# Kernel optimization log

Measured on AMD Instinct MI355X. Metric: run time of the kernel, lower is better.

Reference implementation:

```python
import jax, jax.numpy as jnp
import numpy as np
import math

KSIZE = 5

def setup_inputs() -> dict:
    key = jax.random.key(0)
    ks = jax.random.split(key, 4)
    B, Cp, h, w = 4, 80, 64, 64
    Cf, H, W = 256, 128, 128
    Cc = 64
    pred = jax.random.normal(ks[0], (B, Cp, h, w), dtype=jnp.float32)
    feat = jax.random.normal(ks[1], (B, Cf, H, W), dtype=jnp.float32)
    # hr_compress: 1x1 conv, xavier-like scale; bias zero (matches _reset_parameters)
    w_compress = jax.random.normal(ks[2], (Cc, Cf), dtype=jnp.float32) * (1.0 / np.sqrt(Cf))
    b_compress = jnp.zeros((Cc,), dtype=jnp.float32)
    # content_encoder: 3x3 conv, std=0.001 init; bias zero
    w_enc = jax.random.normal(ks[3], (KSIZE * KSIZE, Cc, 3, 3), dtype=jnp.float32) * 0.001
    b_enc = jnp.zeros((KSIZE * KSIZE,), dtype=jnp.float32)
    return dict(pred=pred, feat=feat, w_compress=w_compress, b_compress=b_compress,
                w_enc=w_enc, b_enc=b_enc)


def _carafe(x, normed_mask, k, up):
    # x: (b, c, h, w) low-res; normed_mask: (b, k*k, H, W) softmax over k*k
    b, c, h, w = x.shape
    _, _, H, W = normed_mask.shape
    pad = k // 2
    px = jnp.pad(x, ((0, 0), (0, 0), (pad, pad), (pad, pad)), mode='reflect')
    # F.unfold ordering: kernel offsets row-major (ki, kj) -> (b, c, k*k, h, w)
    patches = jnp.stack([px[:, :, i:i + h, j:j + w]
                         for i in range(k) for j in range(k)], axis=2)
    # nearest-neighbor upsample by `up` then crop to (H, W): out[i,j] = in[i//up, j//up]
    iy = jnp.arange(H) // up
    ix = jnp.arange(W) // up
    pu = patches[:, :, :, iy[:, None], ix[None, :]]  # (b, c, k*k, H, W)
    return jnp.sum(pu * normed_mask[:, None, :, :, :], axis=2)  # (b, c, H, W)


def reference(pred, feat, w_compress, b_compress, w_enc, b_enc):
    B, Cf, H, W = feat.shape
    _, Cp, h, w = pred.shape
    k = KSIZE
    up = max(math.ceil(H / float(h)), math.ceil(W / float(w)))
    # hr_compress: 1x1 conv as channel contraction
    guide = jnp.einsum('bchw,oc->bohw', feat, w_compress) + b_compress[None, :, None, None]
    # content_encoder: 3x3 SAME conv -> k*k mask logits
    raw = jax.lax.conv_general_dilated(guide, w_enc, (1, 1), 'SAME',
                                       dimension_numbers=('NCHW', 'OIHW', 'NCHW'))
    raw = raw + b_enc[None, :, None, None]
    # kernel normalizer: softmax over the k*k kernel positions (groups=1)
    mask = jax.nn.softmax(raw.reshape(B, 1, k * k, H, W), axis=2).reshape(B, k * k, H, W)
    return _carafe(pred, mask, k, up)
```

## Files before the change

kernel.cpp:

```cpp
#include <hip/hip_runtime.h>
#include <hip/hip_bf16.h>

#define BB   4
#define CF   256
#define CC   64
#define CP   80
#define HH   128
#define WW   128
#define KK   25
#define NPIX 16384

typedef __attribute__((ext_vector_type(8))) short short8v;
typedef __attribute__((ext_vector_type(4))) short short4v;
typedef __attribute__((ext_vector_type(4))) float f32x4;
typedef __attribute__((ext_vector_type(2))) float f32x2;

static __device__ __forceinline__ short f2bf(float f) {
  __hip_bfloat16 h = __float2bfloat16(f);
  return *reinterpret_cast<short*>(&h);
}

__global__ __launch_bounds__(256) void k_compress(
    const float* __restrict__ feat, const float* __restrict__ wc,
    const float* __restrict__ bc, const float* __restrict__ we,
    short* __restrict__ guide, short* __restrict__ webF) {
  __shared__ short Al[32 * 520];
  __shared__ short Bl[64 * 72];
  const int tid = threadIdx.x;
  const int bx = blockIdx.x;
  const int b = bx >> 8;
  const int y = (bx >> 1) & 127;
  const int x0 = (bx & 1) << 6;

  {
    int j = bx * 256 + tid;
    if (j < 9 * 32 * 64) {
      int tap = j >> 11, kk = (j >> 6) & 31, c = j & 63;
      float v = (kk < KK) ? we[(kk * 64 + c) * 9 + tap] : 0.f;
      int c8 = c >> 3, e = c & 7;
      int frag = tap * 4 + ((kk >> 4) << 1) + (c8 >> 2);
      int lane = (kk & 15) | ((c8 & 3) << 4);
      webF[frag * 512 + lane * 8 + e] = f2bf(v);
    }
  }

#pragma unroll
  for (int t = 0; t < 8; ++t) {
    int idx = tid + t * 256;
    int o = idx >> 5, c8 = idx & 31;
    const f32x4* src = (const f32x4*)(wc + o * CF + c8 * 8);
    f32x4 v0 = src[0], v1 = src[1];
    short8v h;
    h[0] = f2bf(v0.x); h[1] = f2bf(v0.y); h[2] = f2bf(v0.z); h[3] = f2bf(v0.w);
    h[4] = f2bf(v1.x); h[5] = f2bf(v1.y); h[6] = f2bf(v1.z); h[7] = f2bf(v1.w);
    int cblk = c8 >> 2, lh4 = c8 & 3;
    *(short8v*)(Al + (cblk * 4 + lh4) * 520 + o * 8) = h;
  }

  const int wave = tid >> 6, l = tid & 63;
  const int l15 = l & 15, lh = l >> 4;
  const int px_s = tid & 63;
  const int c_s = (tid >> 6) << 4;
  const float* fb = feat + (size_t)b * CF * NPIX + y * WW + x0;

  f32x4 acc[4];
#pragma unroll
  for (int m = 0; m < 4; ++m) acc[m] = (f32x4){0.f, 0.f, 0.f, 0.f};

  for (int c0 = 0; c0 < CF; c0 += 64) {
    if (c0) __syncthreads();
    float v[16];
#pragma unroll
    for (int i = 0; i < 16; ++i)
      v[i] = fb[(size_t)(c0 + c_s + i) * NPIX + px_s];
    short8v h0, h1;
#pragma unroll
    for (int e = 0; e < 8; ++e) { h0[e] = f2bf(v[e]); h1[e] = f2bf(v[8 + e]); }
    *(short8v*)(Bl + px_s * 72 + c_s) = h0;
    *(short8v*)(Bl + px_s * 72 + c_s + 8) = h1;
    __syncthreads();
#pragma unroll
    for (int ks = 0; ks < 64; ks += 32) {
      const int cblk = (c0 + ks) >> 5;
      short8v bfr = *(const short8v*)(Bl + (wave * 16 + l15) * 72 + ks + lh * 8);
#pragma unroll
      for (int m = 0; m < 4; ++m) {
        short8v a = *(const short8v*)(Al + (cblk * 4 + lh) * 520 +
                                      (m * 16 + l15) * 8);
        acc[m] = __builtin_amdgcn_mfma_f32_16x16x32_bf16(a, bfr, acc[m], 0, 0, 0);
      }
    }
  }

  const int px = wave * 16 + l15;
  short* gb = guide + ((size_t)((b * HH + y) * WW + x0 + px)) * CC;
#pragma unroll
  for (int m = 0; m < 4; ++m) {
    short4v o;
#pragma unroll
    for (int r = 0; r < 4; ++r) {
      int c = m * 16 + lh * 4 + r;
      o[r] = f2bf(acc[m][r] + bc[c]);
    }
    *(short4v*)(gb + m * 16 + lh * 4) = o;
  }
}

__global__ __launch_bounds__(256, 4) void k_fused(
    const short* __restrict__ guide, const short* __restrict__ webF,
    const float* __restrict__ be, const float* __restrict__ pred,
    float* __restrict__ out) {
  __shared__ char smem[20480];
  short* Gl = (short*)smem;
  float* Ml = (float*)smem;
  float* Pl = (float*)(smem + 7680);
  const int tid = threadIdx.x;
  const int bx = blockIdx.x;
  const int b = bx >> 8;
  const int t = bx & 255;
  const int y0 = (t >> 4) << 3, x0 = (t & 15) << 3;
  const int wave = tid >> 6, l = tid & 63;
  const int l15 = l & 15, lh = l >> 4;

  for (int idx = tid; idx < 10 * 10 * 8; idx += 256) {
    int yp = idx / 80;
    int rem = idx - yp * 80;
    int xp = rem >> 3, cq = (rem & 7) << 3;
    int gy = y0 - 1 + yp, gx = x0 - 1 + xp;
    short8v v = {0, 0, 0, 0, 0, 0, 0, 0};
    if (gy >= 0 && gy < HH && gx >= 0 && gx < WW)
      v = *(const short8v*)(guide + ((size_t)((b * HH + gy) * WW + gx)) * CC + cq);
    *(short8v*)(Gl + (yp * 10 + xp) * 72 + cq) = v;
  }
  __syncthreads();

  const int r_ = wave * 2 + (l15 >> 3);
  const int cx = l15 & 7;
  f32x4 acc0 = {0.f, 0.f, 0.f, 0.f}, acc1 = {0.f, 0.f, 0.f, 0.f};
#pragma unroll
  for (int tap = 0; tap < 9; ++tap) {
    const int dy = tap / 3, dx = tap - dy * 3;
#pragma unroll
    for (int ks32 = 0; ks32 < 2; ++ks32) {
      short8v a0 = *(const short8v*)(webF + (tap * 4 + ks32) * 512 + l * 8);
      short8v a1 = *(const short8v*)(webF + (tap * 4 + 2 + ks32) * 512 + l * 8);
      short8v bf = *(const short8v*)(Gl + ((r_ + dy) * 10 + cx + dx) * 72 +
                                     ks32 * 32 + lh * 8);
      acc0 = __builtin_amdgcn_mfma_f32_16x16x32_bf16(a0, bf, acc0, 0, 0, 0);
      acc1 = __builtin_amdgcn_mfma_f32_16x16x32_bf16(a1, bf, acc1, 0, 0, 0);
    }
  }

  float sv[8];
#pragma unroll
  for (int r = 0; r < 4; ++r) {
    int kk0 = lh * 4 + r;
    sv[r] = acc0[r] + be[kk0];
    int kk1 = 16 + lh * 4 + r;
    sv[4 + r] = (kk1 < KK) ? (acc1[r] + be[kk1]) : -1e30f;
  }
  float mx = sv[0];
#pragma unroll
  for (int i = 1; i < 8; ++i) mx = fmaxf(mx, sv[i]);
  mx = fmaxf(mx, __shfl_xor(mx, 16));
  mx = fmaxf(mx, __shfl_xor(mx, 32));
  float s = 0.f;
#pragma unroll
  for (int i = 0; i < 8; ++i) {
    sv[i] = __expf(sv[i] - mx);
    s += sv[i];
  }
  s += __shfl_xor(s, 16);
  s += __shfl_xor(s, 32);
  float inv = 1.f / s;

  __syncthreads();

  {
    int pxm = wave * 16 + l15;
#pragma unroll
    for (int r = 0; r < 4; ++r) {
      Ml[pxm * 30 + lh * 4 + r] = sv[r] * inv;
      if (lh < 3) Ml[pxm * 30 + 16 + lh * 4 + r] = sv[4 + r] * inv;
    }
  }

  const int g = tid >> 5;
  const int pr = tid & 31;
  const int pry = pr >> 2, prx = pr & 3;
  const int Y = y0 + pry, X = x0 + prx * 2;
  const int ylo = (y0 >> 1) - 2, xlo = (x0 >> 1) - 2;

  float m[2][KK];
  const float* Pbase = Pl + ((pry >> 1) * 8 + prx) * 50 + g * 6;

  for (int half = 0; half < 2; ++half) {
#pragma unroll
    for (int it = 0; it < 10; ++it) {
      int idx = it * 256 + tid;
      int c = idx >> 6;
      int cell = idx & 63;
      int r = cell >> 3, cl = cell & 7;
      int ry = ylo + r;
      ry = ry < 0 ? -ry : (ry > 63 ? 126 - ry : ry);
      int rx = xlo + cl;
      rx = rx < 0 ? -rx : (rx > 63 ? 126 - rx : rx);
      int gg = c / 5, cc = c - gg * 5;
      Pl[cell * 50 + gg * 6 + cc] =
          pred[(((size_t)(b * CP + half * 40 + c)) << 12) + (ry << 6) + rx];
    }
    __syncthreads();

    if (half == 0) {
#pragma unroll
      for (int dxp = 0; dxp < 2; ++dxp) {
        const float* mb = Ml + (pry * 8 + prx * 2 + dxp) * 30;
#pragma unroll
        for (int q = 0; q < 7; ++q) {
          f32x2 lo = *(const f32x2*)(mb + q * 4);
          f32x2 hi = *(const f32x2*)(mb + q * 4 + 2);
          int kk = q * 4;
          m[dxp][kk] = lo.x;
          if (kk + 1 < KK) m[dxp][kk + 1] = lo.y;
          if (kk + 2 < KK) m[dxp][kk + 2] = hi.x;
          if (kk + 3 < KK) m[dxp][kk + 3] = hi.y;
        }
      }
    }

    float acc[5][2];
#pragma unroll
    for (int cc = 0; cc < 5; ++cc) { acc[cc][0] = 0.f; acc[cc][1] = 0.f; }

#pragma unroll
    for (int i = 0; i < 5; ++i)
#pragma unroll
      for (int j = 0; j < 5; ++j) {
        const float* P = Pbase + (i * 8 + j) * 50;
        f32x2 p01 = *(const f32x2*)(P);
        f32x2 p23 = *(const f32x2*)(P + 2);
        float p4 = P[4];
        float m0 = m[0][i * 5 + j], m1 = m[1][i * 5 + j];
        acc[0][0] += p01.x * m0; acc[0][1] += p01.x * m1;
        acc[1][0] += p01.y * m0; acc[1][1] += p01.y * m1;
        acc[2][0] += p23.x * m0; acc[2][1] += p23.x * m1;
        acc[3][0] += p23.y * m0; acc[3][1] += p23.y * m1;
        acc[4][0] += p4    * m0; acc[4][1] += p4    * m1;
      }

#pragma unroll
    for (int cc = 0; cc < 5; ++cc) {
      float* ob = out + (((size_t)(b * CP + half * 40 + g * 5 + cc)) << 14) +
                  Y * WW + X;
      f32x2 v2 = {acc[cc][0], acc[cc][1]};
      *(f32x2*)ob = v2;
    }
    if (half == 0) __syncthreads();
  }
}

extern "C" void kernel_launch(void* const* d_in, const int* in_sizes, int n_in,
                              void* d_out, int out_size, void* d_ws,
                              size_t ws_size, hipStream_t stream) {
  (void)in_sizes; (void)n_in; (void)out_size; (void)ws_size;
  const float* pred = (const float*)d_in[0];
  const float* feat = (const float*)d_in[1];
  const float* wc   = (const float*)d_in[2];
  const float* bc   = (const float*)d_in[3];
  const float* we   = (const float*)d_in[4];
  const float* be   = (const float*)d_in[5];
  float* out = (float*)d_out;

  char* ws = (char*)d_ws;
  short* guide = (short*)ws;
  short* webF  = (short*)(ws + 8388608);

  hipLaunchKernelGGL(k_compress, dim3(1024), dim3(256), 0, stream,
                     feat, wc, bc, we, guide, webF);
  hipLaunchKernelGGL(k_fused, dim3(1024), dim3(256), 0, stream,
                     guide, webF, be, pred, out);
}
```

Measured before the change: 42.94 us.

## Prefetch pred patches into registers to overlap loads with conv and softmax

Moves the global loads of both halves of the pred patch tile into registers earlier in the fused kernel. The first half is issued before the conv/MFMA stage and the second half before the first CARAFE accumulation, so the global-memory latency hides behind compute. The registers are written to LDS only after the earlier data is consumed. This costs 20 extra live floats plus index arrays per thread, which raises register pressure and may lower occupancy, and it adds a barrier around the second-half LDS store.

Measured after the change: 41.73 us. 2.8% less time.

```diff
diff --git a/kernel.cpp b/kernel.cpp
--- a/kernel.cpp
+++ b/kernel.cpp
@@ -132,6 +132,36 @@
       v = *(const short8v*)(guide + ((size_t)((b * HH + gy) * WW + gx)) * CC + cq);
     *(short8v*)(Gl + (yp * 10 + xp) * 72 + cq) = v;
   }
+
+  const int ylo = (y0 >> 1) - 2, xlo = (x0 >> 1) - 2;
+  int pcell[10], pslot[10];
+#pragma unroll
+  for (int it = 0; it < 10; ++it) {
+    int idx = it * 256 + tid;
+    int c = idx >> 6;
+    int cell = idx & 63;
+    int r = cell >> 3, cl = cell & 7;
+    int ry = ylo + r;
+    ry = ry < 0 ? -ry : (ry > 63 ? 126 - ry : ry);
+    int rx = xlo + cl;
+    rx = rx < 0 ? -rx : (rx > 63 ? 126 - rx : rx);
+    int gg = c / 5, cc = c - gg * 5;
+    pcell[it] = cell;
+    pslot[it] = gg * 6 + cc;
+  }
+  float pv0[10];
+#pragma unroll
+  for (int it = 0; it < 10; ++it) {
+    int idx = it * 256 + tid;
+    int c = idx >> 6;
+    int cell = idx & 63;
+    int r = cell >> 3, cl = cell & 7;
+    int ry = ylo + r;
+    ry = ry < 0 ? -ry : (ry > 63 ? 126 - ry : ry);
+    int rx = xlo + cl;
+    rx = rx < 0 ? -rx : (rx > 63 ? 126 - rx : rx);
+    pv0[it] = pred[(((size_t)(b * CP + c)) << 12) + (ry << 6) + rx];
+  }
   __syncthreads();
 
   const int r_ = wave * 2 + (l15 >> 3);
@@ -184,48 +214,54 @@
       if (lh < 3) Ml[pxm * 30 + 16 + lh * 4 + r] = sv[4 + r] * inv;
     }
   }
+#pragma unroll
+  for (int it = 0; it < 10; ++it)
+    Pl[pcell[it] * 50 + pslot[it]] = pv0[it];
+
+  float pv1[10];
+#pragma unroll
+  for (int it = 0; it < 10; ++it) {
+    int idx = it * 256 + tid;
+    int c = idx >> 6;
+    int cell = idx & 63;
+    int r = cell >> 3, cl = cell & 7;
+    int ry = ylo + r;
+    ry = ry < 0 ? -ry : (ry > 63 ? 126 - ry : ry);
+    int rx = xlo + cl;
+    rx = rx < 0 ? -rx : (rx > 63 ? 126 - rx : rx);
+    pv1[it] = pred[(((size_t)(b * CP + 40 + c)) << 12) + (ry << 6) + rx];
+  }
+  __syncthreads();
 
   const int g = tid >> 5;
   const int pr = tid & 31;
   const int pry = pr >> 2, prx = pr & 3;
   const int Y = y0 + pry, X = x0 + prx * 2;
-  const int ylo = (y0 >> 1) - 2, xlo = (x0 >> 1) - 2;
+  const float* Pbase = Pl + ((pry >> 1) * 8 + prx) * 50 + g * 6;
 
   float m[2][KK];
-  const float* Pbase = Pl + ((pry >> 1) * 8 + prx) * 50 + g * 6;
+#pragma unroll
+  for (int dxp = 0; dxp < 2; ++dxp) {
+    const float* mb = Ml + (pry * 8 + prx * 2 + dxp) * 30;
+#pragma unroll
+    for (int q = 0; q < 7; ++q) {
+      f32x2 lo = *(const f32x2*)(mb + q * 4);
+      f32x2 hi = *(const f32x2*)(mb + q * 4 + 2);
+      int kk = q * 4;
+      m[dxp][kk] = lo.x;
+      if (kk + 1 < KK) m[dxp][kk + 1] = lo.y;
+      if (kk + 2 < KK) m[dxp][kk + 2] = hi.x;
+      if (kk + 3 < KK) m[dxp][kk + 3] = hi.y;
+    }
+  }
 
   for (int half = 0; half < 2; ++half) {
-#pragma unroll
-    for (int it = 0; it < 10; ++it) {
-      int idx = it * 256 + tid;
-      int c = idx >> 6;
-      int cell = idx & 63;
-      int r = cell >> 3, cl = cell & 7;
-      int ry = ylo + r;
-      ry = ry < 0 ? -ry : (ry > 63 ? 126 - ry : ry);
-      int rx = xlo + cl;
-      rx = rx < 0 ? -rx : (rx > 63 ? 126 - rx : rx);
-      int gg = c / 5, cc = c - gg * 5;
-      Pl[cell * 50 + gg * 6 + cc] =
-          pred[(((size_t)(b * CP + half * 40 + c)) << 12) + (ry << 6) + rx];
-    }
-    __syncthreads();
-
-    if (half == 0) {
-#pragma unroll
-      for (int dxp = 0; dxp < 2; ++dxp) {
-        const float* mb = Ml + (pry * 8 + prx * 2 + dxp) * 30;
-#pragma unroll
-        for (int q = 0; q < 7; ++q) {
-          f32x2 lo = *(const f32x2*)(mb + q * 4);
-          f32x2 hi = *(const f32x2*)(mb + q * 4 + 2);
-          int kk = q * 4;
-          m[dxp][kk] = lo.x;
-          if (kk + 1 < KK) m[dxp][kk + 1] = lo.y;
-          if (kk + 2 < KK) m[dxp][kk + 2] = hi.x;
-          if (kk + 3 < KK) m[dxp][kk + 3] = hi.y;
-        }
-      }
+    if (half == 1) {
+      __syncthreads();
+#pragma unroll
+      for (int it = 0; it < 10; ++it)
+        Pl[pcell[it] * 50 + pslot[it]] = pv1[it];
+      __syncthreads();
     }
 
     float acc[5][2];
@@ -255,7 +291,6 @@
       f32x2 v2 = {acc[cc][0], acc[cc][1]};
       *(f32x2*)ob = v2;
     }
-    if (half == 0) __syncthreads();
   }
 }
 
```

## Prefetch all pred channels into registers before MFMA and process in one pass

Applied to the files above, without the earlier changes.

Global loads of the whole 80-channel pred halo tile are issued into registers at kernel start, before the guide-tile barrier, so their latency overlaps the 3x3 MFMA encoder and softmax. The two-half pred staging loop is replaced by a single LDS pass (102-float stride) with 10 channels per thread-group, dropping one barrier and the second reload. In exchange, LDS per block grows from 20 KB to about 33 KB and per-thread registers grow (20 prefetch values plus 20 accumulators), which may lower occupancy under launch_bounds(256,4).

After: 42.51 us. Within noise of the previous version (-1.0%).

```diff
diff --git a/kernel.cpp b/kernel.cpp
--- a/kernel.cpp
+++ b/kernel.cpp
@@ -110,7 +110,7 @@
     const short* __restrict__ guide, const short* __restrict__ webF,
     const float* __restrict__ be, const float* __restrict__ pred,
     float* __restrict__ out) {
-  __shared__ char smem[20480];
+  __shared__ char smem[7680 + 26112];
   short* Gl = (short*)smem;
   float* Ml = (float*)smem;
   float* Pl = (float*)(smem + 7680);
@@ -132,6 +132,21 @@
       v = *(const short8v*)(guide + ((size_t)((b * HH + gy) * WW + gx)) * CC + cq);
     *(short8v*)(Gl + (yp * 10 + xp) * 72 + cq) = v;
   }
+
+  const int ylo = (y0 >> 1) - 2, xlo = (x0 >> 1) - 2;
+  float pv[20];
+#pragma unroll
+  for (int it = 0; it < 20; ++it) {
+    int idx = it * 256 + tid;
+    int c = idx >> 6;
+    int cell = idx & 63;
+    int r = cell >> 3, cl = cell & 7;
+    int ry = ylo + r;
+    ry = ry < 0 ? -ry : (ry > 63 ? 126 - ry : ry);
+    int rx = xlo + cl;
+    rx = rx < 0 ? -rx : (rx > 63 ? 126 - rx : rx);
+    pv[it] = pred[(((size_t)(b * CP + c)) << 12) + (ry << 6) + rx];
+  }
   __syncthreads();
 
   const int r_ = wave * 2 + (l15 >> 3);
@@ -184,78 +199,69 @@
       if (lh < 3) Ml[pxm * 30 + 16 + lh * 4 + r] = sv[4 + r] * inv;
     }
   }
+#pragma unroll
+  for (int it = 0; it < 20; ++it) {
+    int idx = it * 256 + tid;
+    int c = idx >> 6;
+    int cell = idx & 63;
+    Pl[cell * 102 + c] = pv[it];
+  }
+  __syncthreads();
 
   const int g = tid >> 5;
   const int pr = tid & 31;
   const int pry = pr >> 2, prx = pr & 3;
   const int Y = y0 + pry, X = x0 + prx * 2;
-  const int ylo = (y0 >> 1) - 2, xlo = (x0 >> 1) - 2;
 
   float m[2][KK];
-  const float* Pbase = Pl + ((pry >> 1) * 8 + prx) * 50 + g * 6;
-
-  for (int half = 0; half < 2; ++half) {
-#pragma unroll
-    for (int it = 0; it < 10; ++it) {
-      int idx = it * 256 + tid;
-      int c = idx >> 6;
-      int cell = idx & 63;
-      int r = cell >> 3, cl = cell & 7;
-      int ry = ylo + r;
-      ry = ry < 0 ? -ry : (ry > 63 ? 126 - ry : ry);
-      int rx = xlo + cl;
-      rx = rx < 0 ? -rx : (rx > 63 ? 126 - rx : rx);
-      int gg = c / 5, cc = c - gg * 5;
-      Pl[cell * 50 + gg * 6 + cc] =
-          pred[(((size_t)(b * CP + half * 40 + c)) << 12) + (ry << 6) + rx];
-    }
-    __syncthreads();
-
-    if (half == 0) {
-#pragma unroll
-      for (int dxp = 0; dxp < 2; ++dxp) {
-        const float* mb = Ml + (pry * 8 + prx * 2 + dxp) * 30;
-#pragma unroll
-        for (int q = 0; q < 7; ++q) {
-          f32x2 lo = *(const f32x2*)(mb + q * 4);
-          f32x2 hi = *(const f32x2*)(mb + q * 4 + 2);
-          int kk = q * 4;
-          m[dxp][kk] = lo.x;
-          if (kk + 1 < KK) m[dxp][kk + 1] = lo.y;
-          if (kk + 2 < KK) m[dxp][kk + 2] = hi.x;
-          if (kk + 3 < KK) m[dxp][kk + 3] = hi.y;
-        }
-      }
-    }
-
-    float acc[5][2];
-#pragma unroll
-    for (int cc = 0; cc < 5; ++cc) { acc[cc][0] = 0.f; acc[cc][1] = 0.f; }
-
-#pragma unroll
-    for (int i = 0; i < 5; ++i)
-#pragma unroll
-      for (int j = 0; j < 5; ++j) {
-        const float* P = Pbase + (i * 8 + j) * 50;
-        f32x2 p01 = *(const f32x2*)(P);
-        f32x2 p23 = *(const f32x2*)(P + 2);
-        float p4 = P[4];
-        float m0 = m[0][i * 5 + j], m1 = m[1][i * 5 + j];
-        acc[0][0] += p01.x * m0; acc[0][1] += p01.x * m1;
-        acc[1][0] += p01.y * m0; acc[1][1] += p01.y * m1;
-        acc[2][0] += p23.x * m0; acc[2][1] += p23.x * m1;
-        acc[3][0] += p23.y * m0; acc[3][1] += p23.y * m1;
-        acc[4][0] += p4    * m0; acc[4][1] += p4    * m1;
-      }
-
-#pragma unroll
-    for (int cc = 0; cc < 5; ++cc) {
-      float* ob = out + (((size_t)(b * CP + half * 40 + g * 5 + cc)) << 14) +
-                  Y * WW + X;
-      f32x2 v2 = {acc[cc][0], acc[cc][1]};
-      *(f32x2*)ob = v2;
-    }
-    if (half == 0) __syncthreads();
+#pragma unroll
+  for (int dxp = 0; dxp < 2; ++dxp) {
+    const float* mb = Ml + (pry * 8 + prx * 2 + dxp) * 30;
+#pragma unroll
+    for (int q = 0; q < 7; ++q) {
+      f32x2 lo = *(const f32x2*)(mb + q * 4);
+      f32x2 hi = *(const f32x2*)(mb + q * 4 + 2);
+      int kk = q * 4;
+      m[dxp][kk] = lo.x;
+      if (kk + 1 < KK) m[dxp][kk + 1] = lo.y;
+      if (kk + 2 < KK) m[dxp][kk + 2] = hi.x;
+      if (kk + 3 < KK) m[dxp][kk + 3] = hi.y;
+    }
+  }
+
+  float acc[10][2];
+#pragma unroll
+  for (int cc = 0; cc < 10; ++cc) { acc[cc][0] = 0.f; acc[cc][1] = 0.f; }
+
+  const float* Pbase = Pl + ((pry >> 1) * 8 + prx) * 102 + g * 10;
+#pragma unroll
+  for (int i = 0; i < 5; ++i)
+#pragma unroll
+    for (int j = 0; j < 5; ++j) {
+      const float* P = Pbase + (i * 8 + j) * 102;
+      f32x2 p01 = *(const f32x2*)(P);
+      f32x2 p23 = *(const f32x2*)(P + 2);
+      f32x2 p45 = *(const f32x2*)(P + 4);
+      f32x2 p67 = *(const f32x2*)(P + 6);
+      f32x2 p89 = *(const f32x2*)(P + 8);
+      float m0 = m[0][i * 5 + j], m1 = m[1][i * 5 + j];
+      acc[0][0] += p01.x * m0; acc[0][1] += p01.x * m1;
+      acc[1][0] += p01.y * m0; acc[1][1] += p01.y * m1;
+      acc[2][0] += p23.x * m0; acc[2][1] += p23.x * m1;
+      acc[3][0] += p23.y * m0; acc[3][1] += p23.y * m1;
+      acc[4][0] += p45.x * m0; acc[4][1] += p45.x * m1;
+      acc[5][0] += p45.y * m0; acc[5][1] += p45.y * m1;
+      acc[6][0] += p67.x * m0; acc[6][1] += p67.x * m1;
+      acc[7][0] += p67.y * m0; acc[7][1] += p67.y * m1;
+      acc[8][0] += p89.x * m0; acc[8][1] += p89.x * m1;
+      acc[9][0] += p89.y * m0; acc[9][1] += p89.y * m1;
+    }
+
+#pragma unroll
+  for (int cc = 0; cc < 10; ++cc) {
+    float* ob = out + (((size_t)(b * CP + g * 10 + cc)) << 14) + Y * WW + X;
+    f32x2 v2 = {acc[cc][0], acc[cc][1]};
+    *(f32x2*)ob = v2;
   }
 }
 
```
